# Optimization experiments

Measured on AMD Instinct MI355X. Metric: run time of the kernel, lower is better.

## Reference

```python
import jax, jax.numpy as jnp
import numpy as np

NUM_NODES = 50000
NUM_EDGES = 50000  # hyperedges
NNZ = 500000       # incidence entries
D_IN = 256
D_OUT = 256


def setup_inputs() -> dict:
    key = jax.random.key(0)
    k1, k2, k3, k4, k5, k6 = jax.random.split(key, 6)
    x = jax.random.normal(k1, (NUM_NODES, D_IN), dtype=jnp.float32)
    node_idx = jax.random.randint(k2, (NNZ,), 0, NUM_NODES, dtype=jnp.int64)
    edge_idx = jax.random.randint(k3, (NNZ,), 0, NUM_EDGES, dtype=jnp.int64)
    hyperedge_index = jnp.stack([node_idx, edge_idx], axis=0)
    hyperedge_weight = jax.random.uniform(k4, (NUM_EDGES,), dtype=jnp.float32)
    # PyG Linear(in, heads*out, bias=False) weight, stored here as [in, out]
    W = jax.random.normal(k5, (D_IN, D_OUT), dtype=jnp.float32) / np.sqrt(D_IN)
    b = jax.random.normal(k6, (D_OUT,), dtype=jnp.float32) * 0.01
    return {"x": x, "hyperedge_index": hyperedge_index,
            "hyperedge_weight": hyperedge_weight, "W": W, "b": b}


def reference(x, hyperedge_index, hyperedge_weight, W, b):
    # PyG HypergraphConv, use_attention=False, heads=1, concat=True:
    #   X' = D^{-1} H B^{-1} H^T (X Theta) + bias, with W folded into D.
    num_nodes = x.shape[0]
    num_edges = hyperedge_weight.shape[0]
    node_idx = hyperedge_index[0]
    edge_idx = hyperedge_index[1]

    xl = x @ W  # [N, F] linear transform (no bias in lin)

    # D[i] = sum over incident hyperedges of their weight; invert, inf -> 0
    D = jax.ops.segment_sum(hyperedge_weight[edge_idx], node_idx,
                            num_segments=num_nodes)
    Dinv = jnp.where(D > 0, 1.0 / D, 0.0)

    # B[e] = hyperedge cardinality; invert, inf -> 0
    Bc = jax.ops.segment_sum(jnp.ones((node_idx.shape[0],), dtype=xl.dtype),
                             edge_idx, num_segments=num_edges)
    Binv = jnp.where(Bc > 0, 1.0 / Bc, 0.0)

    # node -> hyperedge: message = B^{-1}[e] * xl[i], summed per hyperedge
    e_feat = jax.ops.segment_sum(Binv[edge_idx][:, None] * xl[node_idx],
                                 edge_idx, num_segments=num_edges)  # [E, F]

    # hyperedge -> node: message = D^{-1}[i] * e_feat[e], summed per node
    out = jax.ops.segment_sum(Dinv[node_idx][:, None] * e_feat[edge_idx],
                              node_idx, num_segments=num_nodes)  # [N, F]

    return out + b
```

## Files before the change

### kernel.cpp

```cpp
#include <hip/hip_runtime.h>
#include <hip/hip_bf16.h>

#define NUM_NODES 50000
#define NUM_EDGES 50000
#define NNZ       500000
#define D_IN      256
#define D_OUT     256
#define HB        128
#define HW4       12500
#define CHUNK     3907
#define NBLK      196

typedef __attribute__((ext_vector_type(8))) short  bf16x8;
typedef __attribute__((ext_vector_type(4))) float  f32x4;

static __device__ __forceinline__ float bf2f(unsigned short u) {
    return __uint_as_float(((unsigned)u) << 16);
}
static __device__ __forceinline__ unsigned short f2bf(float f) {
    unsigned u = __float_as_uint(f);
    u += 0x7FFFu + ((u >> 16) & 1u);
    return (unsigned short)(u >> 16);
}

__global__ __launch_bounds__(256) void hist_kernel(
    const int* __restrict__ node_idx, const int* __restrict__ edge_idx,
    unsigned int* __restrict__ HbE, unsigned int* __restrict__ HbN,
    const float* __restrict__ W, unsigned short* __restrict__ Wt)
{
    const int arr = blockIdx.y;
    {
        int n = arr * HB + blockIdx.x;
        Wt[n * 256 + threadIdx.x] = f2bf(W[(size_t)threadIdx.x * 256 + n]);
    }
    const int* __restrict__ idx = arr ? node_idx : edge_idx;
    unsigned int* __restrict__ Hb = arr ? HbN : HbE;
    __shared__ unsigned int h[HW4];
    for (int i = threadIdx.x; i < HW4; i += 256) h[i] = 0;
    __syncthreads();
    int beg = blockIdx.x * CHUNK;
    int end = min(NNZ, beg + CHUNK);
    for (int i = beg + (int)threadIdx.x; i < end; i += 256) {
        int k = idx[i];
        atomicAdd(&h[k >> 2], 1u << ((k & 3) * 8));
    }
    __syncthreads();
    unsigned int* out = Hb + (size_t)blockIdx.x * HW4;
    for (int i = threadIdx.x; i < HW4; i += 256) out[i] = h[i];
}

__global__ __launch_bounds__(256) void hreduce_kernel(
    unsigned int* __restrict__ HbE, unsigned int* __restrict__ HbN,
    int* __restrict__ Bc, int* __restrict__ node_cnt)
{
    const int arr = blockIdx.y;
    unsigned int* __restrict__ Hb = arr ? HbN : HbE;
    int* __restrict__ cnt = arr ? node_cnt : Bc;
    int wd = blockIdx.x * 256 + (int)threadIdx.x;
    if (wd >= HW4) return;
    unsigned int s0 = 0, s1 = 0, s2 = 0, s3 = 0;
    #pragma unroll 8
    for (int b = 0; b < HB; ++b) {
        unsigned int u = Hb[(size_t)b * HW4 + wd];
        Hb[(size_t)b * HW4 + wd] = s0 | (s1 << 8) | (s2 << 16) | (s3 << 24);
        s0 += u & 0xffu;
        s1 += (u >> 8) & 0xffu;
        s2 += (u >> 16) & 0xffu;
        s3 += (u >> 24) & 0xffu;
    }
    cnt[4 * wd]     = (int)s0;
    cnt[4 * wd + 1] = (int)s1;
    cnt[4 * wd + 2] = (int)s2;
    cnt[4 * wd + 3] = (int)s3;
}

__global__ __launch_bounds__(256) void scan1_kernel(
    const int* __restrict__ cntE, const int* __restrict__ cntN,
    int* __restrict__ offE, int* __restrict__ offN, int* __restrict__ bsums)
{
    const int arr = blockIdx.y;
    const int* cnt = arr ? cntN : cntE;
    int* off       = arr ? offN : offE;
    int tid = threadIdx.x;
    int i = blockIdx.x * 256 + tid;
    int v = (i < 50000) ? cnt[i] : 0;
    __shared__ int sh[256];
    sh[tid] = v;
    __syncthreads();
    for (int s = 1; s < 256; s <<= 1) {
        int t = (tid >= s) ? sh[tid - s] : 0;
        __syncthreads();
        sh[tid] += t;
        __syncthreads();
    }
    if (i < 50000) off[i] = sh[tid] - v;
    if (tid == 255) bsums[arr * NBLK + blockIdx.x] = sh[255];
}

__global__ __launch_bounds__(256) void scan2_kernel(
    const int* __restrict__ bsums, int* __restrict__ bsum_off,
    int* __restrict__ offE, int* __restrict__ offN)
{
    __shared__ int sh[256];
    int tid = threadIdx.x;
    for (int arr = 0; arr < 2; ++arr) {
        int v = (tid < NBLK) ? bsums[arr * NBLK + tid] : 0;
        sh[tid] = v;
        __syncthreads();
        for (int s = 1; s < 256; s <<= 1) {
            int t = (tid >= s) ? sh[tid - s] : 0;
            __syncthreads();
            sh[tid] += t;
            __syncthreads();
        }
        if (tid < NBLK) bsum_off[arr * NBLK + tid] = sh[tid] - v;
        if (tid == NBLK - 1) {
            int* off = arr ? offN : offE;
            off[50000] = NNZ - (sh[tid] - v);
        }
        __syncthreads();
    }
}

__global__ __launch_bounds__(256) void fill_kernel(
    const int* __restrict__ node_idx, const int* __restrict__ edge_idx,
    const unsigned int* __restrict__ HbE, const unsigned int* __restrict__ HbN,
    const int* __restrict__ edge_off, const int* __restrict__ node_off,
    const int* __restrict__ bsum_off,
    int* __restrict__ edge_nodes, int* __restrict__ node_edges)
{
    const int arr = blockIdx.y;
    const int* __restrict__ key = arr ? node_idx : edge_idx;
    const int* __restrict__ val = arr ? edge_idx : node_idx;
    const unsigned int* __restrict__ Hb = arr ? HbN : HbE;
    const int* __restrict__ off = arr ? node_off : edge_off;
    const int* __restrict__ bs  = bsum_off + arr * NBLK;
    int* __restrict__ out       = arr ? node_edges : edge_nodes;

    __shared__ unsigned int h[HW4];
    const unsigned int* hrow = Hb + (size_t)blockIdx.x * HW4;
    for (int i = threadIdx.x; i < HW4; i += 256) h[i] = hrow[i];
    __syncthreads();

    int beg = blockIdx.x * CHUNK;
    int end = min(NNZ, beg + CHUNK);
    for (int i = beg + (int)threadIdx.x; i < end; i += 256) {
        int k = key[i];
        int sh = (k & 3) * 8;
        unsigned int old = atomicAdd(&h[k >> 2], 1u << sh);
        int rank = (int)((old >> sh) & 0xffu);
        out[off[k] + bs[k >> 8] + rank] = val[i];
    }
}

__global__ __launch_bounds__(256) void gemm_kernel(
    const float* __restrict__ x, const unsigned short* __restrict__ Wt,
    unsigned short* __restrict__ xl)
{
    __shared__ __align__(16) unsigned short sA[32 * 256];
    __shared__ __align__(16) unsigned short sB[2][256 * 32];

    const int tid  = threadIdx.x;
    const int l    = tid & 63;
    const int wq   = tid >> 6;
    const int quad = l >> 4;
    const int l15  = l & 15;
    const int m0   = blockIdx.x * 32;

    {
        int row = tid >> 3;
        int kb  = (tid & 7) * 32;
        int gm = m0 + row; if (gm > NUM_NODES - 1) gm = NUM_NODES - 1;
        const float* p = x + (size_t)gm * D_IN + kb;
        #pragma unroll
        for (int j = 0; j < 4; ++j) {
            float4 v0 = *(const float4*)(p + j * 8);
            float4 v1 = *(const float4*)(p + j * 8 + 4);
            bf16x8 av;
            av[0] = (short)f2bf(v0.x); av[1] = (short)f2bf(v0.y);
            av[2] = (short)f2bf(v0.z); av[3] = (short)f2bf(v0.w);
            av[4] = (short)f2bf(v1.x); av[5] = (short)f2bf(v1.y);
            av[6] = (short)f2bf(v1.z); av[7] = (short)f2bf(v1.w);
            int u  = (kb >> 3) + j;
            int us = u ^ (row & 7);
            *(bf16x8*)(&sA[row * 256 + us * 8]) = av;
        }
    }
    bf16x8 breg[4];
    #pragma unroll
    for (int i = 0; i < 4; ++i) {
        int c = i * 256 + tid, row = c >> 2, g = c & 3;
        breg[i] = *(const bf16x8*)(Wt + row * 256 + g * 8);
    }

    f32x4 acc[2][4];
    #pragma unroll
    for (int i = 0; i < 2; ++i)
        #pragma unroll
        for (int j = 0; j < 4; ++j) acc[i][j] = (f32x4){0.f, 0.f, 0.f, 0.f};

    int buf = 0;
    for (int k0 = 0; k0 < 8; ++k0) {
        #pragma unroll
        for (int i = 0; i < 4; ++i) {
            int c = i * 256 + tid, row = c >> 2, g = c & 3;
            int s = g ^ ((row >> 1) & 3);
            *(bf16x8*)(&sB[buf][row * 32 + s * 8]) = breg[i];
        }
        __syncthreads();
        if (k0 < 7) {
            #pragma unroll
            for (int i = 0; i < 4; ++i) {
                int c = i * 256 + tid, row = c >> 2, g = c & 3;
                breg[i] = *(const bf16x8*)(Wt + row * 256 + (k0 + 1) * 32 + g * 8);
            }
        }
        bf16x8 af[2];
        #pragma unroll
        for (int mi = 0; mi < 2; ++mi) {
            int r  = mi * 16 + l15;
            int us = (k0 * 4 + quad) ^ (r & 7);
            af[mi] = *(const bf16x8*)(&sA[r * 256 + us * 8]);
        }
        bf16x8 bfr[4];
        #pragma unroll
        for (int ni = 0; ni < 4; ++ni) {
            int r = wq * 64 + ni * 16 + l15;
            int s = quad ^ ((r >> 1) & 3);
            bfr[ni] = *(const bf16x8*)(&sB[buf][r * 32 + s * 8]);
        }
        #pragma unroll
        for (int mi = 0; mi < 2; ++mi)
            #pragma unroll
            for (int ni = 0; ni < 4; ++ni)
                acc[mi][ni] = __builtin_amdgcn_mfma_f32_16x16x32_bf16(
                    af[mi], bfr[ni], acc[mi][ni], 0, 0, 0);
        buf ^= 1;
    }

    float* bounce = (float*)&sB[0][0];
    for (int half = 0; half < 2; ++half) {
        __syncthreads();
        #pragma unroll
        for (int ni = 0; ni < 4; ++ni) {
            int col = wq * 64 + ni * 16 + l15;
            #pragma unroll
            for (int r = 0; r < 4; ++r)
                bounce[(quad * 4 + r) * 260 + col] = acc[half][ni][r];
        }
        __syncthreads();
        int row = tid >> 4;
        int c0  = (tid & 15) * 16;
        int gm  = m0 + half * 16 + row;
        if (gm < NUM_NODES) {
            const float* src = bounce + row * 260 + c0;
            bf16x8 o0, o1;
            #pragma unroll
            for (int j = 0; j < 8; ++j) o0[j] = (short)f2bf(src[j]);
            #pragma unroll
            for (int j = 0; j < 8; ++j) o1[j] = (short)f2bf(src[8 + j]);
            *(bf16x8*)(xl + (size_t)gm * D_OUT + c0)     = o0;
            *(bf16x8*)(xl + (size_t)gm * D_OUT + c0 + 8) = o1;
        }
    }
}

__global__ __launch_bounds__(256) void edge_agg_kernel(
    const unsigned short* __restrict__ xl,
    const int* __restrict__ edge_off, const int* __restrict__ bsE,
    const int* __restrict__ edge_nodes,
    unsigned short* __restrict__ e_feat)
{
    int e = blockIdx.x * 4 + (threadIdx.x >> 6);
    int lane = threadIdx.x & 63;
    if (e >= NUM_EDGES) return;
    int beg = edge_off[e]     + bsE[e >> 8];
    int end = edge_off[e + 1] + bsE[(e + 1) >> 8];
    float ax = 0.f, ay = 0.f, az = 0.f, aw = 0.f;
    int j = beg;
    for (; j + 4 <= end; j += 4) {
        int n0 = edge_nodes[j];
        int n1 = edge_nodes[j + 1];
        int n2 = edge_nodes[j + 2];
        int n3 = edge_nodes[j + 3];
        ushort4 u0 = *(const ushort4*)(xl + (size_t)n0 * D_OUT + lane * 4);
        ushort4 u1 = *(const ushort4*)(xl + (size_t)n1 * D_OUT + lane * 4);
        ushort4 u2 = *(const ushort4*)(xl + (size_t)n2 * D_OUT + lane * 4);
        ushort4 u3 = *(const ushort4*)(xl + (size_t)n3 * D_OUT + lane * 4);
        ax += bf2f(u0.x) + bf2f(u1.x) + bf2f(u2.x) + bf2f(u3.x);
        ay += bf2f(u0.y) + bf2f(u1.y) + bf2f(u2.y) + bf2f(u3.y);
        az += bf2f(u0.z) + bf2f(u1.z) + bf2f(u2.z) + bf2f(u3.z);
        aw += bf2f(u0.w) + bf2f(u1.w) + bf2f(u2.w) + bf2f(u3.w);
    }
    for (; j < end; ++j) {
        int node = edge_nodes[j];
        ushort4 u = *(const ushort4*)(xl + (size_t)node * D_OUT + lane * 4);
        ax += bf2f(u.x); ay += bf2f(u.y); az += bf2f(u.z); aw += bf2f(u.w);
    }
    float binv = (end > beg) ? 1.0f / (float)(end - beg) : 0.0f;
    ushort4 o;
    o.x = f2bf(ax * binv); o.y = f2bf(ay * binv);
    o.z = f2bf(az * binv); o.w = f2bf(aw * binv);
    *(ushort4*)(e_feat + (size_t)e * D_OUT + lane * 4) = o;
}

__global__ __launch_bounds__(256) void node_agg_kernel(
    const unsigned short* __restrict__ e_feat,
    const int* __restrict__ node_off, const int* __restrict__ bsN,
    const int* __restrict__ node_edges,
    const float* __restrict__ w, const float* __restrict__ bias,
    float* __restrict__ out)
{
    int n = blockIdx.x * 4 + (threadIdx.x >> 6);
    int lane = threadIdx.x & 63;
    if (n >= NUM_NODES) return;
    int beg = node_off[n]     + bsN[n >> 8];
    int end = node_off[n + 1] + bsN[(n + 1) >> 8];
    float ax = 0.f, ay = 0.f, az = 0.f, aw = 0.f;
    float dsum = 0.f;
    int j = beg;
    for (; j + 4 <= end; j += 4) {
        int e0 = node_edges[j];
        int e1 = node_edges[j + 1];
        int e2 = node_edges[j + 2];
        int e3 = node_edges[j + 3];
        ushort4 u0 = *(const ushort4*)(e_feat + (size_t)e0 * D_OUT + lane * 4);
        ushort4 u1 = *(const ushort4*)(e_feat + (size_t)e1 * D_OUT + lane * 4);
        ushort4 u2 = *(const ushort4*)(e_feat + (size_t)e2 * D_OUT + lane * 4);
        ushort4 u3 = *(const ushort4*)(e_feat + (size_t)e3 * D_OUT + lane * 4);
        dsum += w[e0] + w[e1] + w[e2] + w[e3];
        ax += bf2f(u0.x) + bf2f(u1.x) + bf2f(u2.x) + bf2f(u3.x);
        ay += bf2f(u0.y) + bf2f(u1.y) + bf2f(u2.y) + bf2f(u3.y);
        az += bf2f(u0.z) + bf2f(u1.z) + bf2f(u2.z) + bf2f(u3.z);
        aw += bf2f(u0.w) + bf2f(u1.w) + bf2f(u2.w) + bf2f(u3.w);
    }
    for (; j < end; ++j) {
        int e = node_edges[j];
        dsum += w[e];
        ushort4 u = *(const ushort4*)(e_feat + (size_t)e * D_OUT + lane * 4);
        ax += bf2f(u.x); ay += bf2f(u.y); az += bf2f(u.z); aw += bf2f(u.w);
    }
    float dinv = (dsum > 0.0f) ? 1.0f / dsum : 0.0f;
    float4 bv = *(const float4*)(bias + lane * 4);
    float4 o;
    o.x = ax * dinv + bv.x;
    o.y = ay * dinv + bv.y;
    o.z = az * dinv + bv.z;
    o.w = aw * dinv + bv.w;
    *(float4*)(out + (size_t)n * D_OUT + lane * 4) = o;
}

extern "C" void kernel_launch(void* const* d_in, const int* in_sizes, int n_in,
                              void* d_out, int out_size, void* d_ws, size_t ws_size,
                              hipStream_t stream) {
    const float* x    = (const float*)d_in[0];
    const int*   hidx = (const int*)d_in[1];
    const float* w    = (const float*)d_in[2];
    const float* W    = (const float*)d_in[3];
    const float* b    = (const float*)d_in[4];
    const int* node_idx = hidx;
    const int* edge_idx = hidx + NNZ;

    char* ws = (char*)d_ws;
    size_t off = 0;
    auto alloc = [&](size_t bytes) -> void* {
        off = (off + 511) & ~(size_t)511;
        void* p = ws + off;
        off += bytes;
        return p;
    };
    unsigned short* xl     = (unsigned short*)alloc((size_t)NUM_NODES * D_OUT * 2);
    unsigned short* e_feat = (unsigned short*)alloc((size_t)NUM_EDGES * D_OUT * 2);
    int* Bc         = (int*)alloc(50000 * sizeof(int));
    int* node_cnt   = (int*)alloc(50000 * sizeof(int));
    int* edge_off   = (int*)alloc((NUM_EDGES + 1) * sizeof(int));
    int* node_off   = (int*)alloc((NUM_NODES + 1) * sizeof(int));
    int* edge_nodes = (int*)alloc((size_t)NNZ * sizeof(int));
    int* node_edges = (int*)alloc((size_t)NNZ * sizeof(int));
    unsigned short* Wt = (unsigned short*)alloc(256 * 256 * 2);
    int* bsums    = (int*)alloc(2 * NBLK * sizeof(int));
    int* bsum_off = (int*)alloc(2 * NBLK * sizeof(int));

    unsigned int* HbE = (unsigned int*)xl;
    unsigned int* HbN = (unsigned int*)e_feat;

    hist_kernel<<<dim3(HB, 2), 256, 0, stream>>>(node_idx, edge_idx, HbE, HbN, W, Wt);
    hreduce_kernel<<<dim3((HW4 + 255) / 256, 2), 256, 0, stream>>>(HbE, HbN, Bc, node_cnt);
    scan1_kernel<<<dim3(NBLK, 2), 256, 0, stream>>>(Bc, node_cnt, edge_off, node_off, bsums);
    scan2_kernel<<<1, 256, 0, stream>>>(bsums, bsum_off, edge_off, node_off);
    fill_kernel<<<dim3(HB, 2), 256, 0, stream>>>(node_idx, edge_idx, HbE, HbN,
                                                 edge_off, node_off, bsum_off,
                                                 edge_nodes, node_edges);
    gemm_kernel<<<(NUM_NODES + 31) / 32, 256, 0, stream>>>(x, Wt, xl);
    edge_agg_kernel<<<NUM_EDGES / 4, 256, 0, stream>>>(xl, edge_off, bsum_off,
                                                       edge_nodes, e_feat);
    node_agg_kernel<<<NUM_NODES / 4, 256, 0, stream>>>(e_feat, node_off, bsum_off + NBLK,
                                                       node_edges, w, b, (float*)d_out);
}
```

Before: 241.1 us.

## Fuse histogram reduce into scan and split aggregation kernels across feature halves

Merges the histogram column-reduction into the first scan kernel, so the per-item counts go straight to shared memory and the Bc/node_cnt buffers and one launch are dropped. The edge and node aggregation kernels now launch a second grid dimension that splits the 256 features into two halves, each lane handling 2 features instead of 4. This doubles the number of waves to raise memory-level parallelism on the gather loops. In exchange, the index and weight loads are repeated per half, the loads become narrower, and the reduce now runs on only 64 threads per block.

Measured after the change: 266.5 us. 1.11x slower.

```diff
diff --git a/kernel.cpp b/kernel.cpp
--- a/kernel.cpp
+++ b/kernel.cpp
@@ -49,42 +49,39 @@
     for (int i = threadIdx.x; i < HW4; i += 256) out[i] = h[i];
 }
 
-__global__ __launch_bounds__(256) void hreduce_kernel(
+__global__ __launch_bounds__(256) void hredscan_kernel(
     unsigned int* __restrict__ HbE, unsigned int* __restrict__ HbN,
-    int* __restrict__ Bc, int* __restrict__ node_cnt)
+    int* __restrict__ offE, int* __restrict__ offN, int* __restrict__ bsums)
 {
     const int arr = blockIdx.y;
     unsigned int* __restrict__ Hb = arr ? HbN : HbE;
-    int* __restrict__ cnt = arr ? node_cnt : Bc;
-    int wd = blockIdx.x * 256 + (int)threadIdx.x;
-    if (wd >= HW4) return;
-    unsigned int s0 = 0, s1 = 0, s2 = 0, s3 = 0;
-    #pragma unroll 8
-    for (int b = 0; b < HB; ++b) {
-        unsigned int u = Hb[(size_t)b * HW4 + wd];
-        Hb[(size_t)b * HW4 + wd] = s0 | (s1 << 8) | (s2 << 16) | (s3 << 24);
-        s0 += u & 0xffu;
-        s1 += (u >> 8) & 0xffu;
-        s2 += (u >> 16) & 0xffu;
-        s3 += (u >> 24) & 0xffu;
-    }
-    cnt[4 * wd]     = (int)s0;
-    cnt[4 * wd + 1] = (int)s1;
-    cnt[4 * wd + 2] = (int)s2;
-    cnt[4 * wd + 3] = (int)s3;
-}
-
-__global__ __launch_bounds__(256) void scan1_kernel(
-    const int* __restrict__ cntE, const int* __restrict__ cntN,
-    int* __restrict__ offE, int* __restrict__ offN, int* __restrict__ bsums)
-{
-    const int arr = blockIdx.y;
-    const int* cnt = arr ? cntN : cntE;
-    int* off       = arr ? offN : offE;
-    int tid = threadIdx.x;
-    int i = blockIdx.x * 256 + tid;
-    int v = (i < 50000) ? cnt[i] : 0;
+    int* __restrict__ off = arr ? offN : offE;
     __shared__ int sh[256];
+    const int tid = (int)threadIdx.x;
+    const int b   = (int)blockIdx.x;
+
+    if (tid < 64) {
+        int w = b * 64 + tid;
+        unsigned int s0 = 0, s1 = 0, s2 = 0, s3 = 0;
+        if (w < HW4) {
+            #pragma unroll 8
+            for (int r = 0; r < HB; ++r) {
+                unsigned int u = Hb[(size_t)r * HW4 + w];
+                Hb[(size_t)r * HW4 + w] = s0 | (s1 << 8) | (s2 << 16) | (s3 << 24);
+                s0 += u & 0xffu;
+                s1 += (u >> 8) & 0xffu;
+                s2 += (u >> 16) & 0xffu;
+                s3 += (u >> 24) & 0xffu;
+            }
+        }
+        sh[tid * 4]     = (int)s0;
+        sh[tid * 4 + 1] = (int)s1;
+        sh[tid * 4 + 2] = (int)s2;
+        sh[tid * 4 + 3] = (int)s3;
+    }
+    __syncthreads();
+    int v = sh[tid];
+    __syncthreads();
     sh[tid] = v;
     __syncthreads();
     for (int s = 1; s < 256; s <<= 1) {
@@ -93,8 +90,9 @@
         sh[tid] += t;
         __syncthreads();
     }
+    int i = b * 256 + tid;
     if (i < 50000) off[i] = sh[tid] - v;
-    if (tid == 255) bsums[arr * NBLK + blockIdx.x] = sh[255];
+    if (tid == 255) bsums[arr * NBLK + b] = sh[255];
 }
 
 __global__ __launch_bounds__(256) void scan2_kernel(
@@ -273,35 +271,33 @@
 {
     int e = blockIdx.x * 4 + (threadIdx.x >> 6);
     int lane = threadIdx.x & 63;
+    int fo = blockIdx.y * 128 + lane * 2;
     if (e >= NUM_EDGES) return;
     int beg = edge_off[e]     + bsE[e >> 8];
     int end = edge_off[e + 1] + bsE[(e + 1) >> 8];
-    float ax = 0.f, ay = 0.f, az = 0.f, aw = 0.f;
+    float ax = 0.f, ay = 0.f;
     int j = beg;
     for (; j + 4 <= end; j += 4) {
         int n0 = edge_nodes[j];
         int n1 = edge_nodes[j + 1];
         int n2 = edge_nodes[j + 2];
         int n3 = edge_nodes[j + 3];
-        ushort4 u0 = *(const ushort4*)(xl + (size_t)n0 * D_OUT + lane * 4);
-        ushort4 u1 = *(const ushort4*)(xl + (size_t)n1 * D_OUT + lane * 4);
-        ushort4 u2 = *(const ushort4*)(xl + (size_t)n2 * D_OUT + lane * 4);
-        ushort4 u3 = *(const ushort4*)(xl + (size_t)n3 * D_OUT + lane * 4);
+        ushort2 u0 = *(const ushort2*)(xl + (size_t)n0 * D_OUT + fo);
+        ushort2 u1 = *(const ushort2*)(xl + (size_t)n1 * D_OUT + fo);
+        ushort2 u2 = *(const ushort2*)(xl + (size_t)n2 * D_OUT + fo);
+        ushort2 u3 = *(const ushort2*)(xl + (size_t)n3 * D_OUT + fo);
         ax += bf2f(u0.x) + bf2f(u1.x) + bf2f(u2.x) + bf2f(u3.x);
         ay += bf2f(u0.y) + bf2f(u1.y) + bf2f(u2.y) + bf2f(u3.y);
-        az += bf2f(u0.z) + bf2f(u1.z) + bf2f(u2.z) + bf2f(u3.z);
-        aw += bf2f(u0.w) + bf2f(u1.w) + bf2f(u2.w) + bf2f(u3.w);
     }
     for (; j < end; ++j) {
         int node = edge_nodes[j];
-        ushort4 u = *(const ushort4*)(xl + (size_t)node * D_OUT + lane * 4);
-        ax += bf2f(u.x); ay += bf2f(u.y); az += bf2f(u.z); aw += bf2f(u.w);
+        ushort2 u = *(const ushort2*)(xl + (size_t)node * D_OUT + fo);
+        ax += bf2f(u.x); ay += bf2f(u.y);
     }
     float binv = (end > beg) ? 1.0f / (float)(end - beg) : 0.0f;
-    ushort4 o;
+    ushort2 o;
     o.x = f2bf(ax * binv); o.y = f2bf(ay * binv);
-    o.z = f2bf(az * binv); o.w = f2bf(aw * binv);
-    *(ushort4*)(e_feat + (size_t)e * D_OUT + lane * 4) = o;
+    *(ushort2*)(e_feat + (size_t)e * D_OUT + fo) = o;
 }
 
 __global__ __launch_bounds__(256) void node_agg_kernel(
@@ -313,10 +309,11 @@
 {
     int n = blockIdx.x * 4 + (threadIdx.x >> 6);
     int lane = threadIdx.x & 63;
+    int fo = blockIdx.y * 128 + lane * 2;
     if (n >= NUM_NODES) return;
     int beg = node_off[n]     + bsN[n >> 8];
     int end = node_off[n + 1] + bsN[(n + 1) >> 8];
-    float ax = 0.f, ay = 0.f, az = 0.f, aw = 0.f;
+    float ax = 0.f, ay = 0.f;
     float dsum = 0.f;
     int j = beg;
     for (; j + 4 <= end; j += 4) {
@@ -324,30 +321,26 @@
         int e1 = node_edges[j + 1];
         int e2 = node_edges[j + 2];
         int e3 = node_edges[j + 3];
-        ushort4 u0 = *(const ushort4*)(e_feat + (size_t)e0 * D_OUT + lane * 4);
-        ushort4 u1 = *(const ushort4*)(e_feat + (size_t)e1 * D_OUT + lane * 4);
-        ushort4 u2 = *(const ushort4*)(e_feat + (size_t)e2 * D_OUT + lane * 4);
-        ushort4 u3 = *(const ushort4*)(e_feat + (size_t)e3 * D_OUT + lane * 4);
+        ushort2 u0 = *(const ushort2*)(e_feat + (size_t)e0 * D_OUT + fo);
+        ushort2 u1 = *(const ushort2*)(e_feat + (size_t)e1 * D_OUT + fo);
+        ushort2 u2 = *(const ushort2*)(e_feat + (size_t)e2 * D_OUT + fo);
+        ushort2 u3 = *(const ushort2*)(e_feat + (size_t)e3 * D_OUT + fo);
         dsum += w[e0] + w[e1] + w[e2] + w[e3];
         ax += bf2f(u0.x) + bf2f(u1.x) + bf2f(u2.x) + bf2f(u3.x);
         ay += bf2f(u0.y) + bf2f(u1.y) + bf2f(u2.y) + bf2f(u3.y);
-        az += bf2f(u0.z) + bf2f(u1.z) + bf2f(u2.z) + bf2f(u3.z);
-        aw += bf2f(u0.w) + bf2f(u1.w) + bf2f(u2.w) + bf2f(u3.w);
     }
     for (; j < end; ++j) {
         int e = node_edges[j];
         dsum += w[e];
-        ushort4 u = *(const ushort4*)(e_feat + (size_t)e * D_OUT + lane * 4);
-        ax += bf2f(u.x); ay += bf2f(u.y); az += bf2f(u.z); aw += bf2f(u.w);
+        ushort2 u = *(const ushort2*)(e_feat + (size_t)e * D_OUT + fo);
+        ax += bf2f(u.x); ay += bf2f(u.y);
     }
     float dinv = (dsum > 0.0f) ? 1.0f / dsum : 0.0f;
-    float4 bv = *(const float4*)(bias + lane * 4);
-    float4 o;
+    float2 bv = *(const float2*)(bias + fo);
+    float2 o;
     o.x = ax * dinv + bv.x;
     o.y = ay * dinv + bv.y;
-    o.z = az * dinv + bv.z;
-    o.w = aw * dinv + bv.w;
-    *(float4*)(out + (size_t)n * D_OUT + lane * 4) = o;
+    *(float2*)(out + (size_t)n * D_OUT + fo) = o;
 }
 
 extern "C" void kernel_launch(void* const* d_in, const int* in_sizes, int n_in,
@@ -371,8 +364,6 @@
     };
     unsigned short* xl     = (unsigned short*)alloc((size_t)NUM_NODES * D_OUT * 2);
     unsigned short* e_feat = (unsigned short*)alloc((size_t)NUM_EDGES * D_OUT * 2);
-    int* Bc         = (int*)alloc(50000 * sizeof(int));
-    int* node_cnt   = (int*)alloc(50000 * sizeof(int));
     int* edge_off   = (int*)alloc((NUM_EDGES + 1) * sizeof(int));
     int* node_off   = (int*)alloc((NUM_NODES + 1) * sizeof(int));
     int* edge_nodes = (int*)alloc((size_t)NNZ * sizeof(int));
@@ -385,15 +376,16 @@
     unsigned int* HbN = (unsigned int*)e_feat;
 
     hist_kernel<<<dim3(HB, 2), 256, 0, stream>>>(node_idx, edge_idx, HbE, HbN, W, Wt);
-    hreduce_kernel<<<dim3((HW4 + 255) / 256, 2), 256, 0, stream>>>(HbE, HbN, Bc, node_cnt);
-    scan1_kernel<<<dim3(NBLK, 2), 256, 0, stream>>>(Bc, node_cnt, edge_off, node_off, bsums);
+    hredscan_kernel<<<dim3(NBLK, 2), 256, 0, stream>>>(HbE, HbN, edge_off, node_off, bsums);
     scan2_kernel<<<1, 256, 0, stream>>>(bsums, bsum_off, edge_off, node_off);
     fill_kernel<<<dim3(HB, 2), 256, 0, stream>>>(node_idx, edge_idx, HbE, HbN,
                                                  edge_off, node_off, bsum_off,
                                                  edge_nodes, node_edges);
     gemm_kernel<<<(NUM_NODES + 31) / 32, 256, 0, stream>>>(x, Wt, xl);
-    edge_agg_kernel<<<NUM_EDGES / 4, 256, 0, stream>>>(xl, edge_off, bsum_off,
-                                                       edge_nodes, e_feat);
-    node_agg_kernel<<<NUM_NODES / 4, 256, 0, stream>>>(e_feat, node_off, bsum_off + NBLK,
-                                                       node_edges, w, b, (float*)d_out);
-}
+    edge_agg_kernel<<<dim3(NUM_EDGES / 4, 2), 256, 0, stream>>>(xl, edge_off, bsum_off,
+                                                                edge_nodes, e_feat);
+    node_agg_kernel<<<dim3(NUM_NODES / 4, 2), 256, 0, stream>>>(e_feat, node_off,
+                                                                bsum_off + NBLK,
+                                                                node_edges, w, b,
+                                                                (float*)d_out);
+}
```
